# Optimization experiments

Hardware: AMD Instinct MI355X
Metric: run time of the kernel (lower is better)

The kernel has to match this reference:

```python
import jax, jax.numpy as jnp
import numpy as np
import math

INPUT_SIZE = 1024
OUTPUT_SIZE = 1024
QK_SIZE = 1024
B, S = 4, 2048


def setup_inputs() -> dict:
    key = jax.random.key(0)
    ks = jax.random.split(key, 7)
    scale = 1.0 / math.sqrt(INPUT_SIZE)
    return {
        "x": jax.random.normal(ks[0], (B, S, INPUT_SIZE), dtype=jnp.float32),
        "Wq": jax.random.uniform(ks[1], (QK_SIZE, INPUT_SIZE), minval=-scale, maxval=scale, dtype=jnp.float32),
        "bq": jax.random.uniform(ks[2], (QK_SIZE,), minval=-scale, maxval=scale, dtype=jnp.float32),
        "Wk": jax.random.uniform(ks[3], (QK_SIZE, INPUT_SIZE), minval=-scale, maxval=scale, dtype=jnp.float32),
        "bk": jax.random.uniform(ks[4], (QK_SIZE,), minval=-scale, maxval=scale, dtype=jnp.float32),
        "Wv": jax.random.uniform(ks[5], (OUTPUT_SIZE, INPUT_SIZE), minval=-scale, maxval=scale, dtype=jnp.float32),
        "bv": jax.random.uniform(ks[6], (OUTPUT_SIZE,), minval=-scale, maxval=scale, dtype=jnp.float32),
    }


def reference(x, Wq, bq, Wk, bk, Wv, bv):
    # torch Linear: y = x @ W.T + b
    q = jnp.einsum('bsd,ed->bse', x, Wq) + bq  # [B,S,QK]
    k = jnp.einsum('bsd,ed->bse', x, Wk) + bk  # [B,S,QK]
    v = jnp.einsum('bsd,ed->bse', x, Wv) + bv  # [B,S,OUT]
    inv_sqrt_d = 1.0 / math.sqrt(QK_SIZE)
    scores = jnp.einsum('bqe,bke->bqk', q, k) * inv_sqrt_d  # [B,S,S]
    attn = jax.nn.softmax(scores, axis=-1)
    return jnp.einsum('bqk,bko->bqo', attn, v)  # [B,S,OUT]
```

## Files before the change

### kernel.cpp

```cpp
#include <hip/hip_runtime.h>
#include <stdint.h>

typedef unsigned short u16;
typedef __attribute__((ext_vector_type(8))) __bf16 bf16x8;
typedef __attribute__((ext_vector_type(4))) float f32x4;

__device__ __forceinline__ u16 f2bf(float f) {
    union { float f; uint32_t u; } v; v.f = f;
    uint32_t r = (v.u + 0x7FFFu + ((v.u >> 16) & 1u)) >> 16;
    return (u16)r;
}

__device__ __forceinline__ void lds_fence() {
    __asm__ volatile("s_waitcnt lgkmcnt(0)" ::: "memory");
}

#define BM 128
#define BN 128
#define BK 32

template<int MODE, int PRIV>
__global__ __launch_bounds__(256, 2) void gemm_bt(
    const u16* __restrict__ A, const u16* __restrict__ Bt,
    const float* __restrict__ b0, const float* __restrict__ b1, const float* __restrict__ b2,
    u16* __restrict__ o0, u16* __restrict__ o1, u16* __restrict__ o2,
    float* __restrict__ o3, float* __restrict__ lsum,
    int M, int N, int K, long sA, long sB, long sC, float scale)
{
    __shared__ __align__(16) u16 smem[BM * BK + BN * BK];
    __shared__ __align__(16) u16 epi[PRIV ? 4 * 64 * 72 : 4];
    u16* As = smem;
    u16* Bs = smem + BM * BK;

    const int t = threadIdx.x;
    const int lane = t & 63;
    const int wave = t >> 6;
    const int wm = (wave & 1) * 64;
    const int wn = (wave >> 1) * 64;
    const int bm = blockIdx.y * BM;
    const int bn = blockIdx.x * BN;
    const long bz = blockIdx.z;
    const u16* Ab = A + bz * sA;
    const u16* Bb = Bt + bz * sB;

    f32x4 acc[4][4];
#pragma unroll
    for (int i = 0; i < 4; ++i)
#pragma unroll
        for (int j = 0; j < 4; ++j)
            acc[i][j] = (f32x4){0.f, 0.f, 0.f, 0.f};

    const int lrow = t >> 2;
    const int lcol = (t & 3) * 8;

    for (int k0 = 0; k0 < K; k0 += BK) {
#pragma unroll
        for (int r = 0; r < 2; ++r) {
            const u16* ga = Ab + (long)(bm + r * 64 + lrow) * K + (k0 + lcol);
            __builtin_amdgcn_global_load_lds(
                (const __attribute__((address_space(1))) void*)ga,
                (__attribute__((address_space(3))) void*)&As[(r * 256 + t) * 8],
                16, 0, 0);
        }
#pragma unroll
        for (int r = 0; r < 2; ++r) {
            const u16* gb = Bb + (long)(bn + r * 64 + lrow) * K + (k0 + lcol);
            __builtin_amdgcn_global_load_lds(
                (const __attribute__((address_space(1))) void*)gb,
                (__attribute__((address_space(3))) void*)&Bs[(r * 256 + t) * 8],
                16, 0, 0);
        }
        __syncthreads();

        const int fm = lane & 15;
        const int fk = (lane >> 4) * 8;
        bf16x8 af[4], bfr[4];
#pragma unroll
        for (int i = 0; i < 4; ++i) {
            af[i]  = *(const bf16x8*)&As[(wm + i * 16 + fm) * BK + fk];
            bfr[i] = *(const bf16x8*)&Bs[(wn + i * 16 + fm) * BK + fk];
        }
#pragma unroll
        for (int i = 0; i < 4; ++i)
#pragma unroll
            for (int j = 0; j < 4; ++j)
                acc[i][j] = __builtin_amdgcn_mfma_f32_16x16x32_bf16(af[i], bfr[j], acc[i][j], 0, 0, 0);
        __syncthreads();
    }

    const int cm = (lane >> 4) * 4;
    const int cn = lane & 15;
    u16* Ew = PRIV ? (epi + wave * (64 * 72)) : (smem + wave * 2048);

    if (MODE == 3) {
        float* Fw = (float*)Ew;
#pragma unroll
        for (int p = 0; p < 8; ++p) {
            if (p) lds_fence();
            const int i = p >> 1;
            const int h = p & 1;
            if ((cm & 8) == (h << 3)) {
#pragma unroll
                for (int j = 0; j < 4; ++j)
#pragma unroll
                    for (int r = 0; r < 4; ++r)
                        Fw[((cm & 7) + r) * 68 + j * 16 + cn] = acc[i][j][r];
            }
#pragma unroll
            for (int it = 0; it < 2; ++it) {
                const int rl = it * 4 + (lane >> 4);
                const int c4 = (lane & 15) * 4;
                f32x4 w = *(const f32x4*)&Fw[rl * 68 + c4];
                const int gm = bm + wm + i * 16 + h * 8 + rl;
                const float inv = __builtin_amdgcn_rcpf(lsum[bz * 2048 + gm]);
                w[0] *= inv; w[1] *= inv; w[2] *= inv; w[3] *= inv;
                *(f32x4*)&o3[bz * sC + (long)gm * N + bn + wn + c4] = w;
            }
        }
    } else if (MODE == 0 && (bn >> 10) == 2) {
        float bb[4];
#pragma unroll
        for (int j = 0; j < 4; ++j) bb[j] = b2[(bn & 1023) + wn + j * 16 + cn];
        const int bgi = (bm + wm) >> 11;
        const int sbase = (bm + wm) & 2047;
#pragma unroll
        for (int i = 0; i < 4; ++i)
#pragma unroll
            for (int j = 0; j < 4; ++j) {
                ushort4 pk;
                pk.x = f2bf(acc[i][j][0] + bb[j]);
                pk.y = f2bf(acc[i][j][1] + bb[j]);
                pk.z = f2bf(acc[i][j][2] + bb[j]);
                pk.w = f2bf(acc[i][j][3] + bb[j]);
                *(ushort4*)&Ew[(j * 16 + cn) * 72 + i * 16 + cm] = pk;
            }
#pragma unroll
        for (int it = 0; it < 8; ++it) {
            const int e = it * 8 + (lane >> 3);
            const int s8 = (lane & 7) * 8;
            const uint4 w = *(const uint4*)&Ew[e * 72 + s8];
            const int eg = (bn & 1023) + wn + e;
            *(uint4*)&o2[((((long)bgi << 10) + eg) << 11) + sbase + s8] = w;
        }
    } else if (MODE == 0) {
        const int sec = bn >> 10;
        u16* C = sec ? o1 : o0;
        const float* bias = sec ? b1 : b0;
        const int ncol0 = bn & 1023;
        float bb[4];
#pragma unroll
        for (int j = 0; j < 4; ++j) bb[j] = bias[ncol0 + wn + j * 16 + cn];
#pragma unroll
        for (int i = 0; i < 4; ++i)
#pragma unroll
            for (int j = 0; j < 4; ++j) {
                const int col = j * 16 + cn;
#pragma unroll
                for (int r = 0; r < 4; ++r)
                    Ew[(i * 16 + cm + r) * 72 + col] = f2bf(acc[i][j][r] + bb[j]);
            }
#pragma unroll
        for (int it = 0; it < 8; ++it) {
            const int row = it * 8 + (lane >> 3);
            const int c8 = (lane & 7) * 8;
            const uint4 w = *(const uint4*)&Ew[row * 72 + c8];
            const int gm = bm + wm + row;
            *(uint4*)&C[(long)gm * 1024 + ncol0 + wn + c8] = w;
        }
    } else {
#pragma unroll
        for (int i = 0; i < 4; ++i)
#pragma unroll
            for (int j = 0; j < 4; ++j)
#pragma unroll
                for (int r = 0; r < 4; ++r)
                    acc[i][j][r] = __expf(acc[i][j][r] * scale);
#pragma unroll
        for (int i = 0; i < 4; ++i) {
#pragma unroll
            for (int r = 0; r < 4; ++r) {
                float s = acc[i][0][r] + acc[i][1][r] + acc[i][2][r] + acc[i][3][r];
                s += __shfl_xor(s, 1);
                s += __shfl_xor(s, 2);
                s += __shfl_xor(s, 4);
                s += __shfl_xor(s, 8);
                if (cn == 0)
                    atomicAdd(&lsum[bz * 2048 + bm + wm + i * 16 + cm + r], s);
            }
        }
#pragma unroll
        for (int i = 0; i < 4; ++i) {
            if (i) lds_fence();
#pragma unroll
            for (int j = 0; j < 4; ++j) {
                const int col = j * 16 + cn;
#pragma unroll
                for (int r = 0; r < 4; ++r)
                    Ew[(cm + r) * 72 + col] = f2bf(acc[i][j][r]);
            }
#pragma unroll
            for (int it = 0; it < 2; ++it) {
                const int rl = it * 8 + (lane >> 3);
                const int c8 = (lane & 7) * 8;
                const uint4 w = *(const uint4*)&Ew[rl * 72 + c8];
                const int gm = bm + wm + i * 16 + rl;
                *(uint4*)&o0[bz * sC + (long)gm * N + bn + wn + c8] = w;
            }
        }
    }
}

__global__ __launch_bounds__(256) void cvt_all(
    const float* __restrict__ x, const float* __restrict__ wq,
    const float* __restrict__ wk, const float* __restrict__ wv,
    u16* __restrict__ xb, u16* __restrict__ wb, float* __restrict__ lsum)
{
    const int b = blockIdx.x;
    if (b >= 11264) {
        const long i = (long)(b - 11264) * 1024 + threadIdx.x * 4;
        *(f32x4*)(lsum + i) = (f32x4){0.f, 0.f, 0.f, 0.f};
        return;
    }
    const float* src; u16* dst; long base;
    if (b < 8192)       { src = x;  dst = xb;             base = (long)b * 1024; }
    else if (b < 9216)  { src = wq; dst = wb;             base = (long)(b - 8192) * 1024; }
    else if (b < 10240) { src = wk; dst = wb + (1 << 20); base = (long)(b - 9216) * 1024; }
    else                { src = wv; dst = wb + (2 << 20); base = (long)(b - 10240) * 1024; }
    const long i = base + threadIdx.x * 4;
    const f32x4 f = *(const f32x4*)(src + i);
    ushort4 o;
    o.x = f2bf(f[0]); o.y = f2bf(f[1]); o.z = f2bf(f[2]); o.w = f2bf(f[3]);
    *(ushort4*)(dst + i) = o;
}

extern "C" void kernel_launch(void* const* d_in, const int* in_sizes, int n_in,
                              void* d_out, int out_size, void* d_ws, size_t ws_size,
                              hipStream_t stream) {
    const float* x  = (const float*)d_in[0];
    const float* Wq = (const float*)d_in[1];
    const float* bq = (const float*)d_in[2];
    const float* Wk = (const float*)d_in[3];
    const float* bk = (const float*)d_in[4];
    const float* Wv = (const float*)d_in[5];
    const float* bv = (const float*)d_in[6];
    float* out = (float*)d_out;

    const int B = 4, S = 2048, D = 1024, E = 1024;
    const int M = B * S;

    u16* xb  = (u16*)d_ws;
    u16* wb  = xb  + (size_t)M * D;
    u16* qb  = wb  + (size_t)3 * E * D;
    u16* kb  = qb  + (size_t)M * E;
    u16* vbT = kb  + (size_t)M * E;
    u16* sb  = vbT + (size_t)M * E;
    float* lsum = (float*)(sb + (size_t)M * S);

    cvt_all<<<11272, 256, 0, stream>>>(x, Wq, Wk, Wv, xb, wb, lsum);

    dim3 blk(256);
    gemm_bt<0, 1><<<dim3(3 * E / BN, M / BM, 1), blk, 0, stream>>>(
        xb, wb, bq, bk, bv, qb, kb, vbT, nullptr, nullptr, M, 3 * E, D, 0, 0, 0, 1.f);
    gemm_bt<2, 0><<<dim3(S / BN, S / BM, B), blk, 0, stream>>>(
        qb, kb, nullptr, nullptr, nullptr, sb, nullptr, nullptr, nullptr, lsum,
        S, S, E, (long)S * E, (long)S * E, (long)S * S, 0.03125f);
    gemm_bt<3, 0><<<dim3(E / BN, S / BM, B), blk, 0, stream>>>(
        sb, vbT, nullptr, nullptr, nullptr, nullptr, nullptr, nullptr, out, lsum,
        S, E, S, (long)S * S, (long)E * S, (long)S * E, 1.f);
}
```

Before: 260.3 us.

## Double GEMM K-tile to 64, unify LDS buffer, and batch epilogue stores

Measured after the change: 241.8 us. 1.08x faster.

```diff
diff --git a/kernel.cpp b/kernel.cpp
--- a/kernel.cpp
+++ b/kernel.cpp
@@ -17,20 +17,17 @@
 
 #define BM 128
 #define BN 128
-#define BK 32
-
-template<int MODE, int PRIV>
-__global__ __launch_bounds__(256, 2) void gemm_bt(
+#define BK 64
+
+template<int MODE>
+__global__ __launch_bounds__(256, 4) void gemm_bt(
     const u16* __restrict__ A, const u16* __restrict__ Bt,
     const float* __restrict__ b0, const float* __restrict__ b1, const float* __restrict__ b2,
     u16* __restrict__ o0, u16* __restrict__ o1, u16* __restrict__ o2,
     float* __restrict__ o3, float* __restrict__ lsum,
     int M, int N, int K, long sA, long sB, long sC, float scale)
 {
-    __shared__ __align__(16) u16 smem[BM * BK + BN * BK];
-    __shared__ __align__(16) u16 epi[PRIV ? 4 * 64 * 72 : 4];
-    u16* As = smem;
-    u16* Bs = smem + BM * BK;
+    __shared__ __align__(16) u16 smem[4 * 64 * 72];
 
     const int t = threadIdx.x;
     const int lane = t & 63;
@@ -52,66 +49,73 @@
 
     const int lrow = t >> 2;
     const int lcol = (t & 3) * 8;
+    const int fm = lane & 15;
+    const int fk = (lane >> 4) * 8;
 
     for (int k0 = 0; k0 < K; k0 += BK) {
 #pragma unroll
-        for (int r = 0; r < 2; ++r) {
-            const u16* ga = Ab + (long)(bm + r * 64 + lrow) * K + (k0 + lcol);
-            __builtin_amdgcn_global_load_lds(
-                (const __attribute__((address_space(1))) void*)ga,
-                (__attribute__((address_space(3))) void*)&As[(r * 256 + t) * 8],
-                16, 0, 0);
-        }
-#pragma unroll
-        for (int r = 0; r < 2; ++r) {
-            const u16* gb = Bb + (long)(bn + r * 64 + lrow) * K + (k0 + lcol);
-            __builtin_amdgcn_global_load_lds(
-                (const __attribute__((address_space(1))) void*)gb,
-                (__attribute__((address_space(3))) void*)&Bs[(r * 256 + t) * 8],
-                16, 0, 0);
-        }
+        for (int h = 0; h < 2; ++h)
+#pragma unroll
+            for (int r = 0; r < 2; ++r) {
+                const u16* ga = Ab + (long)(bm + r * 64 + lrow) * K + (k0 + h * 32 + lcol);
+                __builtin_amdgcn_global_load_lds(
+                    (const __attribute__((address_space(1))) void*)ga,
+                    (__attribute__((address_space(3))) void*)&smem[h * 4096 + (r * 256 + t) * 8],
+                    16, 0, 0);
+            }
+#pragma unroll
+        for (int h = 0; h < 2; ++h)
+#pragma unroll
+            for (int r = 0; r < 2; ++r) {
+                const u16* gb = Bb + (long)(bn + r * 64 + lrow) * K + (k0 + h * 32 + lcol);
+                __builtin_amdgcn_global_load_lds(
+                    (const __attribute__((address_space(1))) void*)gb,
+                    (__attribute__((address_space(3))) void*)&smem[8192 + h * 4096 + (r * 256 + t) * 8],
+                    16, 0, 0);
+            }
         __syncthreads();
 
-        const int fm = lane & 15;
-        const int fk = (lane >> 4) * 8;
-        bf16x8 af[4], bfr[4];
-#pragma unroll
-        for (int i = 0; i < 4; ++i) {
-            af[i]  = *(const bf16x8*)&As[(wm + i * 16 + fm) * BK + fk];
-            bfr[i] = *(const bf16x8*)&Bs[(wn + i * 16 + fm) * BK + fk];
-        }
-#pragma unroll
-        for (int i = 0; i < 4; ++i)
-#pragma unroll
-            for (int j = 0; j < 4; ++j)
-                acc[i][j] = __builtin_amdgcn_mfma_f32_16x16x32_bf16(af[i], bfr[j], acc[i][j], 0, 0, 0);
+#pragma unroll
+        for (int h = 0; h < 2; ++h) {
+            bf16x8 af[4], bfr[4];
+#pragma unroll
+            for (int i = 0; i < 4; ++i) {
+                af[i]  = *(const bf16x8*)&smem[h * 4096 + (wm + i * 16 + fm) * 32 + fk];
+                bfr[i] = *(const bf16x8*)&smem[8192 + h * 4096 + (wn + i * 16 + fm) * 32 + fk];
+            }
+#pragma unroll
+            for (int i = 0; i < 4; ++i)
+#pragma unroll
+                for (int j = 0; j < 4; ++j)
+                    acc[i][j] = __builtin_amdgcn_mfma_f32_16x16x32_bf16(af[i], bfr[j], acc[i][j], 0, 0, 0);
+        }
         __syncthreads();
     }
 
     const int cm = (lane >> 4) * 4;
     const int cn = lane & 15;
-    u16* Ew = PRIV ? (epi + wave * (64 * 72)) : (smem + wave * 2048);
+    u16* Ew = smem + wave * 4608;
 
     if (MODE == 3) {
         float* Fw = (float*)Ew;
 #pragma unroll
-        for (int p = 0; p < 8; ++p) {
+        for (int p = 0; p < 2; ++p) {
             if (p) lds_fence();
-            const int i = p >> 1;
-            const int h = p & 1;
-            if ((cm & 8) == (h << 3)) {
+#pragma unroll
+            for (int ii = 0; ii < 2; ++ii) {
+                const int i = p * 2 + ii;
 #pragma unroll
                 for (int j = 0; j < 4; ++j)
 #pragma unroll
                     for (int r = 0; r < 4; ++r)
-                        Fw[((cm & 7) + r) * 68 + j * 16 + cn] = acc[i][j][r];
-            }
-#pragma unroll
-            for (int it = 0; it < 2; ++it) {
-                const int rl = it * 4 + (lane >> 4);
+                        Fw[(ii * 16 + cm + r) * 68 + j * 16 + cn] = acc[i][j][r];
+            }
+#pragma unroll
+            for (int it = 0; it < 8; ++it) {
+                const int row = it * 4 + (lane >> 4);
                 const int c4 = (lane & 15) * 4;
-                f32x4 w = *(const f32x4*)&Fw[rl * 68 + c4];
-                const int gm = bm + wm + i * 16 + h * 8 + rl;
+                f32x4 w = *(const f32x4*)&Fw[row * 68 + c4];
+                const int gm = bm + wm + p * 32 + row;
                 const float inv = __builtin_amdgcn_rcpf(lsum[bz * 2048 + gm]);
                 w[0] *= inv; w[1] *= inv; w[2] *= inv; w[3] *= inv;
                 *(f32x4*)&o3[bz * sC + (long)gm * N + bn + wn + c4] = w;
@@ -189,23 +193,21 @@
             }
         }
 #pragma unroll
-        for (int i = 0; i < 4; ++i) {
-            if (i) lds_fence();
+        for (int i = 0; i < 4; ++i)
 #pragma unroll
             for (int j = 0; j < 4; ++j) {
                 const int col = j * 16 + cn;
 #pragma unroll
                 for (int r = 0; r < 4; ++r)
-                    Ew[(cm + r) * 72 + col] = f2bf(acc[i][j][r]);
-            }
-#pragma unroll
-            for (int it = 0; it < 2; ++it) {
-                const int rl = it * 8 + (lane >> 3);
-                const int c8 = (lane & 7) * 8;
-                const uint4 w = *(const uint4*)&Ew[rl * 72 + c8];
-                const int gm = bm + wm + i * 16 + rl;
-                *(uint4*)&o0[bz * sC + (long)gm * N + bn + wn + c8] = w;
-            }
+                    Ew[(i * 16 + cm + r) * 72 + col] = f2bf(acc[i][j][r]);
+            }
+#pragma unroll
+        for (int it = 0; it < 8; ++it) {
+            const int row = it * 8 + (lane >> 3);
+            const int c8 = (lane & 7) * 8;
+            const uint4 w = *(const uint4*)&Ew[row * 72 + c8];
+            const int gm = bm + wm + row;
+            *(uint4*)&o0[bz * sC + (long)gm * N + bn + wn + c8] = w;
         }
     }
 }
@@ -259,12 +261,12 @@
     cvt_all<<<11272, 256, 0, stream>>>(x, Wq, Wk, Wv, xb, wb, lsum);
 
     dim3 blk(256);
-    gemm_bt<0, 1><<<dim3(3 * E / BN, M / BM, 1), blk, 0, stream>>>(
+    gemm_bt<0><<<dim3(3 * E / BN, M / BM, 1), blk, 0, stream>>>(
         xb, wb, bq, bk, bv, qb, kb, vbT, nullptr, nullptr, M, 3 * E, D, 0, 0, 0, 1.f);
-    gemm_bt<2, 0><<<dim3(S / BN, S / BM, B), blk, 0, stream>>>(
+    gemm_bt<2><<<dim3(S / BN, S / BM, B), blk, 0, stream>>>(
         qb, kb, nullptr, nullptr, nullptr, sb, nullptr, nullptr, nullptr, lsum,
         S, S, E, (long)S * E, (long)S * E, (long)S * S, 0.03125f);
-    gemm_bt<3, 0><<<dim3(E / BN, S / BM, B), blk, 0, stream>>>(
+    gemm_bt<3><<<dim3(E / BN, S / BM, B), blk, 0, stream>>>(
         sb, vbT, nullptr, nullptr, nullptr, nullptr, nullptr, nullptr, out, lsum,
         S, E, S, (long)S * S, (long)E * S, (long)S * E, 1.f);
 }
```
